# Performance work log

Hardware: AMD Instinct MI355X
Metric: run time of the kernel (lower is better)

## Reference

```python
import jax, jax.numpy as jnp
import numpy as np

B, L, D = 512, 200, 128
N_ITEMS = 50001
T_STEPS = 4
TAU = 2.0
STEP = 1
V_TH = 1.0
SG_ALPHA = 4.0  # spikingjelly default surrogate.Sigmoid alpha


@jax.custom_vjp
def spike(x):
    return (x >= 0.0).astype(x.dtype)

def _spike_fwd(x):
    return spike(x), x

def _spike_bwd(x, g):
    s = jax.nn.sigmoid(SG_ALPHA * x)
    return (g * SG_ALPHA * s * (1.0 - s),)

spike.defvjp(_spike_fwd, _spike_bwd)


def lif_multistep(x):
    """Multi-step LIF (hard reset to 0, detach_reset). x: [T, ...] -> spikes [T, ...]."""
    def step(v, xt):
        v = v + (xt - v) / TAU  # charge (v_reset = 0)
        s = spike(v - V_TH)
        v = v - jax.lax.stop_gradient(s) * v  # hard reset, detached spike
        return v, s
    v0 = jnp.zeros_like(x[0])
    _, spikes = jax.lax.scan(step, v0, x)
    return spikes


def layernorm(x, g, b, eps=1e-5):
    m = x.mean(-1, keepdims=True)
    v = x.var(-1, keepdims=True)
    return (x - m) / jnp.sqrt(v + eps) * g + b


def _build_session_graphs(rng):
    lens = rng.integers(50, L + 1, size=B)
    item_seq = np.zeros((B, L), dtype=np.int64)
    for b in range(B):
        item_seq[b, :lens[b]] = rng.integers(1, N_ITEMS, size=lens[b])
    alias = np.zeros((B, L), dtype=np.int64)
    items = np.zeros((B, L), dtype=np.int64)
    A = np.zeros((B, L, 2 * L), dtype=np.float32)
    for b in range(B):
        u = item_seq[b]
        node = np.unique(u)  # sorted
        items[b, :len(node)] = node
        alias[b] = np.searchsorted(node, u)
        uA = np.zeros((L, L), dtype=np.float32)
        for i in range(L - 1):
            if u[i + 1] == 0:
                break
            r = np.searchsorted(node, u[i])
            c = np.searchsorted(node, u[i + 1])
            uA[r, c] = 1.0
        sin = uA.sum(0); sin[sin == 0] = 1.0
        sout = uA.sum(1); sout[sout == 0] = 1.0
        A[b, :, :L] = (uA / sin).T          # u_A_in.T
        A[b, :, L:] = ((uA.T / sout)).T     # u_A_out.T
    mask = item_seq > 0
    return A, alias, items, mask, lens.astype(np.int64)


def setup_inputs() -> dict:
    rng = np.random.default_rng(0)
    A, alias, items, mask, lens = _build_session_graphs(rng)
    stdv = 1.0 / np.sqrt(D)
    key = jax.random.key(0)
    ks = jax.random.split(key, 24)
    u = lambda k, shape: jax.random.uniform(k, shape, jnp.float32, -stdv, stdv)
    item_emb = u(ks[0], (N_ITEMS, D)).at[0].set(0.0)  # padding_idx=0
    return {
        "A": jnp.asarray(A),
        "alias_inputs": jnp.asarray(alias),
        "items": jnp.asarray(items),
        "mask": jnp.asarray(mask),
        "item_seq_len": jnp.asarray(lens),
        "item_emb": item_emb,
        "W_in": u(ks[1], (D, D)), "b_in": u(ks[2], (D,)),
        "W_out": u(ks[3], (D, D)), "b_out": u(ks[4], (D,)),
        "w_ih": u(ks[5], (3 * D, 2 * D)), "w_hh": u(ks[6], (3 * D, D)),
        "b_ih": u(ks[7], (3 * D,)), "b_hh": u(ks[8], (3 * D,)),
        "b_iah": u(ks[9], (D,)), "b_ioh": u(ks[10], (D,)),
        "W1": u(ks[11], (D, D)), "W2": u(ks[12], (D, D)),
        "W3": u(ks[13], (1, D)), "Wt": u(ks[14], (D, 2 * D)),
        "g_q": u(ks[15], (D,)), "beta_q": u(ks[16], (D,)),
        "g_sh": u(ks[17], (2 * D,)), "beta_sh": u(ks[18], (2 * D,)),
    }


def _forward(A, alias_inputs, items, mask, item_seq_len, item_emb,
             W_in, b_in, W_out, b_out, w_ih, w_hh, b_ih, b_hh, b_iah, b_ioh,
             W1, W2, W3, Wt, g_q, beta_q, g_sh, beta_sh):
    hidden = item_emb[items]  # [B,L,D]
    for _ in range(STEP):
        ein = hidden @ W_in.T + b_in
        eout = hidden @ W_out.T + b_out
        input_in = jnp.einsum('bij,bjd->bid', A[:, :, :L], ein) + b_iah
        input_out = jnp.einsum('bij,bjd->bid', A[:, :, L:], eout) + b_ioh
        inputs = jnp.concatenate([input_in, input_out], axis=-1)  # [B,L,2D]
        gi = inputs @ w_ih.T + b_ih  # [B,L,3D]
        gh = hidden @ w_hh.T + b_hh
        i_r, i_i, i_n = jnp.split(gi, 3, axis=-1)
        h_r, h_i, h_n = jnp.split(gh, 3, axis=-1)
        r = jax.nn.sigmoid(i_r + h_r)
        z = jax.nn.sigmoid(i_i + h_i)
        n = jnp.tanh(i_n + r * h_n)
        hidden = (1.0 - z) * hidden + z * n
    seq_hidden = jnp.take_along_axis(hidden, alias_inputs[..., None], axis=1)  # [B,L,D]
    ht = jnp.take_along_axis(seq_hidden, (item_seq_len - 1)[:, None, None], axis=1)[:, 0]  # [B,D]
    Qb = (ht @ W1.T)[:, None, :] + seq_hidden @ W2.T  # [B,L,D]
    Q = jnp.broadcast_to(Qb[None], (T_STEPS, B, L, D))
    Qs = lif_multistep(layernorm(Q, g_q, beta_q))
    alpha = Qs @ W3.T  # [T,B,L,1]
    mf = mask.astype(alpha.dtype)
    a = jnp.sum(alpha * seq_hidden[None] * mf[None, :, :, None], axis=2)  # [T,B,D]
    ht_T = jnp.broadcast_to(ht[None], (T_STEPS, B, D))
    sh = jnp.concatenate([a, ht_T], axis=-1)  # [T,B,2D]
    sh = layernorm(lif_multistep(sh), g_sh, beta_sh)
    return (sh @ Wt.T).mean(0)  # [B,D]


def reference(A, alias_inputs, items, mask, item_seq_len, item_emb,
              W_in, b_in, W_out, b_out, w_ih, w_hh, b_ih, b_hh, b_iah, b_ioh,
              W1, W2, W3, Wt, g_q, beta_q, g_sh, beta_sh):
    return _forward(A, alias_inputs, items, mask, item_seq_len, item_emb,
                    W_in, b_in, W_out, b_out, w_ih, w_hh, b_ih, b_hh, b_iah, b_ioh,
                    W1, W2, W3, Wt, g_q, beta_q, g_sh, beta_sh)
```

## Files before the change

kernel.cpp:

```cpp
#include <hip/hip_runtime.h>
#include <hip/hip_bf16.h>
#include <cstdint>
#include <cstddef>

#define B_ 512
#define L_ 200
#define D_ 128
#define M_ (B_*L_)
#define T_ 4

typedef short bf16x8 __attribute__((ext_vector_type(8)));
typedef unsigned short u16x8 __attribute__((ext_vector_type(8)));
typedef float f32x4 __attribute__((ext_vector_type(4)));

__device__ __forceinline__ float bf2f(unsigned short u){
  union { unsigned int i; float f; } c; c.i = ((unsigned int)u)<<16; return c.f;
}
__device__ __forceinline__ unsigned short f2bf(float f){
  union { float f; unsigned int i; } c; c.f = f;
  unsigned int r = c.i + 0x7FFFu + ((c.i>>16)&1u);
  return (unsigned short)(r>>16);
}
__device__ __forceinline__ float wsum(float v){
  #pragma unroll
  for (int m=1;m<64;m<<=1) v += __shfl_xor(v, m, 64);
  return v;
}
__device__ __forceinline__ void gload_lds16(const void* g, void* l){
  __builtin_amdgcn_global_load_lds(
      (const __attribute__((address_space(1))) void*)g,
      (__attribute__((address_space(3))) void*)l, 16, 0, 0);
}

__global__ __launch_bounds__(256)
void gemm_bt(const unsigned short* __restrict__ A, int lda,
             const unsigned short* __restrict__ Bt, int ldb,
             const float* __restrict__ bias,
             unsigned short* __restrict__ C, int ldc, int K,
             const int* __restrict__ mlimit)
{
  const int m0 = blockIdx.y * 128;
  if (mlimit && m0 >= *mlimit) return;
  __shared__ __align__(16) short sAs[2][128*32];
  __shared__ __align__(16) short sBs[2][128*32];
  const int tid = threadIdx.x;
  const int n0 = blockIdx.x * 128;
  const int lane = tid & 63;
  const int w = tid >> 6;
  const int wr = (w>>1)*64, wc = (w&1)*64;

  f32x4 acc[4][4];
  #pragma unroll
  for (int i=0;i<4;i++)
    #pragma unroll
    for (int j=0;j<4;j++) acc[i][j] = (f32x4){0.f,0.f,0.f,0.f};

  const int c1 = tid, c2 = tid + 256;
  const int r1 = c1>>2, s1 = c1&3, k1 = ((s1 ^ ((r1>>1)&3))&3)<<3;
  const int r2 = c2>>2, s2 = c2&3, k2 = ((s2 ^ ((r2>>1)&3))&3)<<3;
  const int fr = lane & 15;
  const int fq = lane >> 4;
  const int fk = ((fq ^ ((fr>>1)&3))&3)<<3;

  auto stage = [&](int t){
    const int buf = t & 1, ks = t << 5;
    gload_lds16(A  + (size_t)(m0 + r1)*lda + ks + k1, sAs[buf] + (size_t)c1*8);
    gload_lds16(A  + (size_t)(m0 + r2)*lda + ks + k2, sAs[buf] + (size_t)c2*8);
    gload_lds16(Bt + (size_t)(n0 + r1)*ldb + ks + k1, sBs[buf] + (size_t)c1*8);
    gload_lds16(Bt + (size_t)(n0 + r2)*ldb + ks + k2, sBs[buf] + (size_t)c2*8);
  };
  const int nT = K >> 5;
  stage(0);
  __syncthreads();
  for (int t=0; t<nT; ++t){
    if (t+1 < nT) stage(t+1);
    const short* a_ = sAs[t&1];
    const short* b_ = sBs[t&1];
    bf16x8 af[4], bfr[4];
    #pragma unroll
    for (int i=0;i<4;i++){
      af[i]  = *(const bf16x8*)(a_ + (wr + i*16 + fr)*32 + fk);
      bfr[i] = *(const bf16x8*)(b_ + (wc + i*16 + fr)*32 + fk);
    }
    #pragma unroll
    for (int i=0;i<4;i++)
      #pragma unroll
      for (int j=0;j<4;j++)
        acc[i][j] = __builtin_amdgcn_mfma_f32_16x16x32_bf16(af[i], bfr[j], acc[i][j], 0,0,0);
    __syncthreads();
  }

  const int orow = fq<<2;
  #pragma unroll
  for (int i=0;i<4;i++){
    #pragma unroll
    for (int j=0;j<4;j++){
      const int gn = n0 + wc + j*16 + fr;
      const float bv = bias ? bias[gn] : 0.f;
      #pragma unroll
      for (int v=0;v<4;v++){
        const int gm = m0 + wr + i*16 + orow + v;
        C[(size_t)gm*ldc + gn] = f2bf(acc[i][j][v] + bv);
      }
    }
  }
}

__global__ __launch_bounds__(128)
void k_prepW(const float* __restrict__ w_ih, const float* __restrict__ w_hh,
             const float* __restrict__ W_in, const float* __restrict__ W_out,
             const float* __restrict__ b_in, const float* __restrict__ b_out,
             const float* __restrict__ b_ih, const float* __restrict__ b_hh,
             const float* __restrict__ b_iah, const float* __restrict__ b_ioh,
             unsigned short* __restrict__ Wbig, float* __restrict__ biasBase,
             float* __restrict__ uIn, float* __restrict__ uOut)
{
  const int p = blockIdx.x, t = threadIdx.x;
  const int dim = p>>2, g = p&3;
  const int row = (g==0) ? dim : (g==1) ? 128+dim : 256+dim;
  const bool has_ih = (g!=3), has_hh = (g!=2);
  __shared__ float wl[128], wrg[128], red[3][128];
  wl[t]  = has_ih ? w_ih[(size_t)row*256 + t]       : 0.f;
  wrg[t] = has_ih ? w_ih[(size_t)row*256 + 128 + t] : 0.f;
  __syncthreads();
  float cin = 0.f, cout = 0.f;
  if (has_ih) {
    for (int m=0;m<128;m++){
      cin  += wl[m]  * W_in [m*128 + t];
      cout += wrg[m] * W_out[m*128 + t];
    }
  }
  Wbig[(size_t)p*384 +       t] = f2bf(cin);
  Wbig[(size_t)p*384 + 128 + t] = f2bf(cout);
  Wbig[(size_t)p*384 + 256 + t] = f2bf(has_hh ? w_hh[(size_t)row*128 + t] : 0.f);
  red[0][t] = wl[t]*b_iah[t] + wrg[t]*b_ioh[t];
  red[1][t] = wl[t]*b_in[t];
  red[2][t] = wrg[t]*b_out[t];
  __syncthreads();
  if (t == 0) {
    float v=0.f, ui=0.f, uo=0.f;
    for (int k=0;k<128;k++){ v += red[0][k]; ui += red[1][k]; uo += red[2][k]; }
    float bb;
    if (g==0)      bb = b_ih[dim]     + b_hh[dim]     + v;
    else if (g==1) bb = b_ih[128+dim] + b_hh[128+dim] + v;
    else if (g==2) bb = b_ih[256+dim] + v;
    else           bb = b_hh[256+dim];
    biasBase[p] = bb;
    uIn[p]  = has_ih ? ui : 0.f;
    uOut[p] = has_ih ? uo : 0.f;
  }
}

__global__ __launch_bounds__(256)
void k_prepSmall(const float* __restrict__ W1, const float* __restrict__ W2,
                 unsigned short* __restrict__ w1b, unsigned short* __restrict__ w2b)
{
  const int i = blockIdx.x*256 + threadIdx.x;
  if (i < 16384) { w1b[i] = f2bf(W1[i]); w2b[i] = f2bf(W2[i]); }
}

__global__ __launch_bounds__(64)
void k_nb(const int* __restrict__ alias, const int* __restrict__ lens,
          int* __restrict__ nb)
{
  const int b = blockIdx.x, lane = threadIdx.x;
  const int len = lens[b];
  int m = 0;
  for (int l=lane; l<len; l+=64) m = max(m, alias[b*L_ + l]);
  #pragma unroll
  for (int o=1;o<64;o<<=1) m = max(m, __shfl_xor(m, o, 64));
  if (lane==0) nb[b] = m + 1;
}

__global__ __launch_bounds__(512)
void k_scan(const int* __restrict__ nb, const int* __restrict__ lens,
            int* __restrict__ nbase, int* __restrict__ vbase)
{
  __shared__ int A[2][512], Bv[2][512];
  const int t = threadIdx.x;
  const int a0 = nb[t], b0 = lens[t];
  A[0][t] = a0; Bv[0][t] = b0;
  __syncthreads();
  int cur = 0;
  for (int off=1; off<512; off<<=1){
    const int nxt = cur^1;
    A[nxt][t]  = A[cur][t]  + (t>=off ? A[cur][t-off]  : 0);
    Bv[nxt][t] = Bv[cur][t] + (t>=off ? Bv[cur][t-off] : 0);
    __syncthreads();
    cur = nxt;
  }
  nbase[t] = A[cur][t] - a0;
  vbase[t] = Bv[cur][t] - b0;
  if (t==511){ nbase[512] = A[cur][511]; vbase[512] = Bv[cur][511]; }
}

__global__ __launch_bounds__(1024)
void k_aggemb(const int* __restrict__ alias, const int* __restrict__ items,
              const int* __restrict__ lens, const float* __restrict__ emb,
              const int* __restrict__ nb, const int* __restrict__ nbase,
              unsigned short* __restrict__ X3, unsigned char* __restrict__ cf)
{
  const int b = blockIdx.x, tid = threadIdx.x;
  __shared__ unsigned short hl[L_*128];
  __shared__ int al[L_], it[L_];
  __shared__ unsigned bmIn[L_*8], bmOut[L_*8];
  if (tid < L_) { al[tid] = alias[b*L_ + tid]; it[tid] = items[b*L_ + tid]; }
  for (int i=tid; i<L_*8; i+=1024){ bmIn[i]=0u; bmOut[i]=0u; }
  __syncthreads();
  const int len = lens[b], nB = nb[b], base = nbase[b];
  if (tid < len-1) {
    const int r = al[tid], c = al[tid+1];
    atomicOr(&bmIn[c*8 + (r>>5)],  1u<<(r&31));
    atomicOr(&bmOut[r*8 + (c>>5)], 1u<<(c&31));
  }
  const int rr = tid>>5, cc = (tid&31)<<2;
  for (int s=0; s<nB; s+=32) {
    const int j = s + rr;
    if (j < nB) {
      const float4 v = *(const float4*)(emb + (size_t)it[j]*128 + cc);
      ushort4 o; o.x=f2bf(v.x); o.y=f2bf(v.y); o.z=f2bf(v.z); o.w=f2bf(v.w);
      *(ushort4*)(hl + j*128 + cc) = o;
      *(ushort4*)(X3 + (size_t)(base + j)*384 + 256 + cc) = o;
    }
  }
  __syncthreads();
  const int g = tid >> 7, d = tid & 127;
  for (int s=0; s<nB; s+=8) {
    const int i = s + g;
    if (i < nB) {
      float si=0.f, so=0.f; int ci=0, co=0;
      #pragma unroll
      for (int wd=0; wd<8; ++wd) {
        unsigned word = bmIn[i*8+wd];
        while (word) { int j = __ffs(word)-1; word &= word-1u;
          si += bf2f(hl[(wd*32+j)*128 + d]); ci++; }
        word = bmOut[i*8+wd];
        while (word) { int j = __ffs(word)-1; word &= word-1u;
          so += bf2f(hl[(wd*32+j)*128 + d]); co++; }
      }
      unsigned short* xr = X3 + (size_t)(base + i)*384;
      xr[d]       = f2bf(si / (float)(ci>0?ci:1));
      xr[128 + d] = f2bf(so / (float)(co>0?co:1));
      if (d == 0) cf[base + i] = (unsigned char)((ci>0?1:0) | (co>0?2:0));
    }
  }
}

__global__ __launch_bounds__(512)
void k_gates_gru(const unsigned short* __restrict__ X3,
                 const unsigned short* __restrict__ Wbig,
                 const float* __restrict__ biasBase,
                 const float* __restrict__ uIn,
                 const float* __restrict__ uOut,
                 const unsigned char* __restrict__ cf,
                 unsigned short* __restrict__ hidden,
                 const int* __restrict__ mlimit)
{
  const int m0 = blockIdx.y * 128;
  if (m0 >= *mlimit) return;
  __shared__ __align__(16) short sA[2][128*32];
  __shared__ __align__(16) short sB[2][256*32];
  const int tid = threadIdx.x;
  const int p0 = blockIdx.x * 256;
  const int lane = tid & 63;
  const int w = tid >> 6;
  const int wr  = (w>>2)*64;
  const int wcp = (w&3)*64;
  const int fr = lane & 15;
  const int fq = lane >> 4;
  const int fk = ((fq ^ ((fr>>1)&3))&3)<<3;

  f32x4 acc[4][4];
  #pragma unroll
  for (int i=0;i<4;i++)
    #pragma unroll
    for (int j=0;j<4;j++) acc[i][j] = (f32x4){0.f,0.f,0.f,0.f};

  const int ra = tid>>2, sa_ = tid&3, ka = ((sa_ ^ ((ra>>1)&3))&3)<<3;
  const int c1 = tid + 512, rb1 = c1>>2, sb1 = c1&3, kb1 = ((sb1 ^ ((rb1>>1)&3))&3)<<3;

  auto stage = [&](int t){
    const int buf = t & 1, ks = t << 5;
    gload_lds16(X3   + (size_t)(m0 + ra )*384 + ks + ka , sA[buf] + (size_t)tid*8);
    gload_lds16(Wbig + (size_t)(p0 + ra )*384 + ks + ka , sB[buf] + (size_t)tid*8);
    gload_lds16(Wbig + (size_t)(p0 + rb1)*384 + ks + kb1, sB[buf] + (size_t)(c1-512)*8 + 512*8);
  };
  stage(0);
  __syncthreads();
  for (int t=0; t<12; ++t){
    if (t < 11) stage(t+1);
    const short* a_ = sA[t&1];
    const short* b_ = sB[t&1];
    bf16x8 af[4], bfr[4];
    #pragma unroll
    for (int i=0;i<4;i++){
      af[i]  = *(const bf16x8*)(a_ + (wr  + i*16 + fr)*32 + fk);
      bfr[i] = *(const bf16x8*)(b_ + (wcp + i*16 + fr)*32 + fk);
    }
    #pragma unroll
    for (int i=0;i<4;i++)
      #pragma unroll
      for (int j=0;j<4;j++)
        acc[i][j] = __builtin_amdgcn_mfma_f32_16x16x32_bf16(af[i], bfr[j], acc[i][j], 0,0,0);
    __syncthreads();
  }

  const bool q0b = (lane & 1), q1b = (lane & 2);
  #pragma unroll
  for (int j=0;j<4;j++){
    const int dim = (p0>>2) + (w&3)*16 + j*4 + ((lane>>2)&3);
    const float4 bb = *(const float4*)(biasBase + dim*4);
    const float4 bi = *(const float4*)(uIn  + dim*4);
    const float4 bo = *(const float4*)(uOut + dim*4);
    #pragma unroll
    for (int i=0;i<4;i++){
      const float a0=acc[i][j][0], a1=acc[i][j][1], a2=acc[i][j][2], a3=acc[i][j][3];
      const float t0=__shfl_xor(a0,1), t1=__shfl_xor(a1,1), t2=__shfl_xor(a2,1), t3=__shfl_xor(a3,1);
      const float s0 = q0b? t1:a0, s1 = q0b? a1:t0, s2 = q0b? t3:a2, s3 = q0b? a3:t2;
      const float u0=__shfl_xor(s0,2), u1=__shfl_xor(s1,2), u2=__shfl_xor(s2,2), u3=__shfl_xor(s3,2);
      float G0 = q1b? u2:s0, G1 = q1b? u3:s1, G2 = q1b? s2:u0, G3 = q1b? s3:u1;
      const int row = m0 + wr + i*16 + fq*4 + (lane&3);
      const unsigned c = cf[row];
      const float fi = (c&1) ? 1.f : 0.f, fo = (c&2) ? 1.f : 0.f;
      G0 += bb.x + fi*bi.x + fo*bo.x;
      G1 += bb.y + fi*bi.y + fo*bo.y;
      G2 += bb.z + fi*bi.z + fo*bo.z;
      G3 += bb.w;
      const float h = bf2f(X3[(size_t)row*384 + 256 + dim]);
      const float r = 1.f/(1.f+__expf(-G0));
      const float z = 1.f/(1.f+__expf(-G1));
      const float x = G2 + r*G3;
      const float n = 1.f - 2.f/(__expf(2.f*x)+1.f);
      hidden[(size_t)row*128 + dim] = f2bf((1.f-z)*h + z*n);
    }
  }
}

__global__ __launch_bounds__(256)
void k_gather(const unsigned short* __restrict__ hidden,
              const int* __restrict__ alias, const int* __restrict__ lens,
              const int* __restrict__ nbase, const int* __restrict__ vbase,
              unsigned short* __restrict__ seqv, unsigned short* __restrict__ htb)
{
  const int idx = blockIdx.x*256 + threadIdx.x;
  const int row = idx >> 4, d8 = (idx & 15) << 3;
  const int b = row / L_, l = row - b*L_;
  const int len = lens[b];
  if (l >= len) return;
  u16x8 v = *(const u16x8*)(hidden + (size_t)(nbase[b] + alias[row])*128 + d8);
  *(u16x8*)(seqv + (size_t)(vbase[b] + l)*128 + d8) = v;
  if (l == len-1) *(u16x8*)(htb + (size_t)b*128 + d8) = v;
}

__global__ __launch_bounds__(1024)
void k_attn(const unsigned short* __restrict__ Q0, const unsigned short* __restrict__ htW1,
            const unsigned short* __restrict__ seqv, const int* __restrict__ lens,
            const int* __restrict__ vbase,
            const float* __restrict__ g_q, const float* __restrict__ beta_q,
            const float* __restrict__ W3, float* __restrict__ a_out)
{
  const int b = blockIdx.x, tid = threadIdx.x;
  const int w = tid>>6, lane = tid&63;
  __shared__ float a_acc[16][T_][128];
  for (int i=tid; i<16*T_*128; i+=1024) ((float*)a_acc)[i] = 0.f;
  const float h0 = bf2f(htW1[b*128 + lane]), h1 = bf2f(htW1[b*128 + lane + 64]);
  const float gq0 = g_q[lane], gq1 = g_q[lane+64];
  const float bq0 = beta_q[lane], bq1 = beta_q[lane+64];
  const float w30 = W3[lane], w31 = W3[lane+64];
  const int len = lens[b], vb = vbase[b];
  __syncthreads();
  for (int l = w; l < len; l += 16) {
    const size_t row = (size_t)(vb + l);
    const float q0 = bf2f(Q0[row*128 + lane]) + h0;
    const float q1 = bf2f(Q0[row*128 + lane + 64]) + h1;
    const float m = wsum(q0+q1) * (1.f/128.f);
    const float d0 = q0-m, d1 = q1-m;
    const float var = wsum(d0*d0 + d1*d1) * (1.f/128.f);
    const float inv = rsqrtf(var + 1e-5f);
    const float x0 = d0*inv*gq0 + bq0;
    const float x1 = d1*inv*gq1 + bq1;
    const float sh0 = bf2f(seqv[row*128+lane]), sh1 = bf2f(seqv[row*128+lane+64]);
    float v0=0.f, v1=0.f;
    #pragma unroll
    for (int t=0;t<T_;t++){
      v0 = 0.5f*(v0+x0); v1 = 0.5f*(v1+x1);
      const float s0 = (v0>=1.f)?1.f:0.f, s1 = (v1>=1.f)?1.f:0.f;
      v0 -= s0*v0; v1 -= s1*v1;
      const float alpha = wsum(s0*w30 + s1*w31);
      a_acc[w][t][lane] += alpha*sh0; a_acc[w][t][lane+64] += alpha*sh1;
    }
  }
  __syncthreads();
  for (int i=tid; i<T_*128; i+=1024){
    const int t = i>>7, d = i&127;
    float s = 0.f;
    #pragma unroll
    for (int p=0;p<16;p++) s += a_acc[p][t][d];
    a_out[((size_t)t*B_ + b)*128 + d] = s;
  }
}

__global__ __launch_bounds__(256)
void k_final(const float* __restrict__ a_in, const unsigned short* __restrict__ hidden,
             const int* __restrict__ alias, const int* __restrict__ lens,
             const int* __restrict__ nbase,
             const float* __restrict__ g_sh, const float* __restrict__ beta_sh,
             const float* __restrict__ Wt, float* __restrict__ out)
{
  const int b = blockIdx.x, tid = threadIdx.x;
  const int w = tid>>6, lane = tid&63;
  __shared__ float ys[256];
  __shared__ float part[T_][4];
  const int len = lens[b];
  float xh = 0.f;
  if (tid >= 128) {
    const int al = alias[b*L_ + len - 1];
    xh = bf2f(hidden[((size_t)(nbase[b] + al))*128 + (tid-128)]);
  }
  float v = 0.f; float sp[T_];
  #pragma unroll
  for (int t=0;t<T_;t++){
    const float x = (tid<128) ? a_in[((size_t)t*B_ + b)*128 + tid] : xh;
    v = 0.5f*(v + x);
    const float s = (v>=1.f)?1.f:0.f;
    v -= s*v;
    sp[t] = s;
  }
  #pragma unroll
  for (int t=0;t<T_;t++){
    const float r = wsum(sp[t]);
    if (lane==0) part[t][w] = r;
  }
  __syncthreads();
  float acc4 = 0.f;
  #pragma unroll
  for (int t=0;t<T_;t++){
    const float k = part[t][0]+part[t][1]+part[t][2]+part[t][3];
    const float mean = k * (1.f/256.f);
    const float varr = mean - mean*mean;
    const float inv = rsqrtf(varr + 1e-5f);
    acc4 += (sp[t]-mean)*inv;
  }
  ys[tid] = acc4*g_sh[tid] + 4.f*beta_sh[tid];
  __syncthreads();
  if (tid < 128) {
    float acc = 0.f;
    const float4* wr4 = (const float4*)(Wt + (size_t)tid*256);
    const float4* ys4 = (const float4*)ys;
    #pragma unroll 8
    for (int k=0;k<64;k++){
      const float4 wv = wr4[k], yv = ys4[k];
      acc += wv.x*yv.x + wv.y*yv.y + wv.z*yv.z + wv.w*yv.w;
    }
    out[(size_t)b*128 + tid] = acc*0.25f;
  }
}

extern "C" void kernel_launch(void* const* d_in, const int* in_sizes, int n_in,
                              void* d_out, int out_size, void* d_ws, size_t ws_size,
                              hipStream_t stream)
{
  const int*   alias  = (const int*)d_in[1];
  const int*   items  = (const int*)d_in[2];
  const int*   lens   = (const int*)d_in[4];
  const float* emb    = (const float*)d_in[5];
  const float* W_in   = (const float*)d_in[6];
  const float* b_in   = (const float*)d_in[7];
  const float* W_out  = (const float*)d_in[8];
  const float* b_out  = (const float*)d_in[9];
  const float* w_ih   = (const float*)d_in[10];
  const float* w_hh   = (const float*)d_in[11];
  const float* b_ih   = (const float*)d_in[12];
  const float* b_hh   = (const float*)d_in[13];
  const float* b_iah  = (const float*)d_in[14];
  const float* b_ioh  = (const float*)d_in[15];
  const float* W1     = (const float*)d_in[16];
  const float* W2     = (const float*)d_in[17];
  const float* W3     = (const float*)d_in[18];
  const float* Wt     = (const float*)d_in[19];
  const float* g_q    = (const float*)d_in[20];
  const float* beta_q = (const float*)d_in[21];
  const float* g_sh   = (const float*)d_in[22];
  const float* beta_sh= (const float*)d_in[23];

  char* ws = (char*)d_ws;
  size_t off = 0;
  auto alloc = [&](size_t bytes)->void* {
    void* p = ws + off; off += (bytes + 255) & ~(size_t)255; return p;
  };
  unsigned short* X3    = (unsigned short*)alloc((size_t)M_*384*2);
  unsigned short* hidden= (unsigned short*)alloc((size_t)M_*128*2);
  unsigned short* seqv  = (unsigned short*)alloc((size_t)M_*128*2);
  unsigned short* Q0c   = (unsigned short*)alloc((size_t)M_*128*2);
  unsigned short* htb   = (unsigned short*)alloc((size_t)B_*128*2);
  unsigned short* htW1  = (unsigned short*)alloc((size_t)B_*128*2);
  float*          a_buf = (float*)alloc((size_t)T_*B_*128*4);
  unsigned short* Wbig  = (unsigned short*)alloc((size_t)512*384*2);
  unsigned short* w1b   = (unsigned short*)alloc(16384*2);
  unsigned short* w2b   = (unsigned short*)alloc(16384*2);
  float*          biasBase = (float*)alloc(512*4);
  float*          uIn   = (float*)alloc(512*4);
  float*          uOut  = (float*)alloc(512*4);
  unsigned char*  cf    = (unsigned char*)alloc(M_);
  int*            nb    = (int*)alloc(512*4);
  int*            nbase = (int*)alloc(513*4);
  int*            vbase = (int*)alloc(513*4);
  if (off > ws_size) return;

  k_prepW<<<512,128,0,stream>>>(w_ih,w_hh,W_in,W_out,b_in,b_out,b_ih,b_hh,
                                b_iah,b_ioh,Wbig,biasBase,uIn,uOut);
  k_prepSmall<<<64,256,0,stream>>>(W1,W2,w1b,w2b);
  k_nb<<<B_,64,0,stream>>>(alias, lens, nb);
  k_scan<<<1,512,0,stream>>>(nb, lens, nbase, vbase);
  k_aggemb<<<B_,1024,0,stream>>>(alias, items, lens, emb, nb, nbase, X3, cf);
  k_gates_gru<<<dim3(2,800),512,0,stream>>>(X3, Wbig, biasBase, uIn, uOut, cf,
                                            hidden, nbase+512);
  k_gather<<<M_*16/256,256,0,stream>>>(hidden, alias, lens, nbase, vbase, seqv, htb);
  gemm_bt<<<dim3(1,4),256,0,stream>>>(htb, 128, w1b, 128, nullptr, htW1, 128, 128, nullptr);
  gemm_bt<<<dim3(1,800),256,0,stream>>>(seqv, 128, w2b, 128, nullptr, Q0c, 128, 128, vbase+512);
  k_attn<<<B_,1024,0,stream>>>(Q0c, htW1, seqv, lens, vbase, g_q, beta_q, W3, a_buf);
  k_final<<<B_,256,0,stream>>>(a_buf, hidden, alias, lens, nbase, g_sh, beta_sh, Wt, (float*)d_out);
}
```

Before: 199.6 us.

## Fuse Q0 GEMM with layernorm/LIF epilogue and triple-buffer GRU GEMM

The W2 GEMM over seqv now computes the layernorm, LIF spikes and alpha projection in its epilogue, so the bf16 Q0 intermediate is never written or reread. The old per-batch attention kernel becomes a light weighted-sum kernel that reads the per-row alpha values. Supporting this, the gather kernel records each row's batch index. Separately, the GRU gates GEMM moves from double to triple-buffered LDS loads with explicit vmcnt waits and one barrier per k-step, to overlap loads with MFMA work. The cost is more LDS per block, an extra alpha buffer in global memory, and hand-written waitcnt logic that must exactly match how many loads are in flight.

```diff
diff --git a/kernel.cpp b/kernel.cpp
--- a/kernel.cpp
+++ b/kernel.cpp
@@ -24,6 +24,11 @@
 __device__ __forceinline__ float wsum(float v){
   #pragma unroll
   for (int m=1;m<64;m<<=1) v += __shfl_xor(v, m, 64);
+  return v;
+}
+__device__ __forceinline__ float rsum16(float v){
+  #pragma unroll
+  for (int m=1;m<16;m<<=1) v += __shfl_xor(v, m, 64);
   return v;
 }
 __device__ __forceinline__ void gload_lds16(const void* g, void* l){
@@ -258,8 +263,8 @@
 {
   const int m0 = blockIdx.y * 128;
   if (m0 >= *mlimit) return;
-  __shared__ __align__(16) short sA[2][128*32];
-  __shared__ __align__(16) short sB[2][256*32];
+  __shared__ __align__(16) short sA[3*128*32];
+  __shared__ __align__(16) short sB[3*256*32];
   const int tid = threadIdx.x;
   const int p0 = blockIdx.x * 256;
   const int lane = tid & 63;
@@ -280,17 +285,20 @@
   const int c1 = tid + 512, rb1 = c1>>2, sb1 = c1&3, kb1 = ((sb1 ^ ((rb1>>1)&3))&3)<<3;
 
   auto stage = [&](int t){
-    const int buf = t & 1, ks = t << 5;
-    gload_lds16(X3   + (size_t)(m0 + ra )*384 + ks + ka , sA[buf] + (size_t)tid*8);
-    gload_lds16(Wbig + (size_t)(p0 + ra )*384 + ks + ka , sB[buf] + (size_t)tid*8);
-    gload_lds16(Wbig + (size_t)(p0 + rb1)*384 + ks + kb1, sB[buf] + (size_t)(c1-512)*8 + 512*8);
+    const int buf = t % 3, ks = t << 5;
+    gload_lds16(X3   + (size_t)(m0 + ra )*384 + ks + ka , sA + buf*4096 + (size_t)tid*8);
+    gload_lds16(Wbig + (size_t)(p0 + ra )*384 + ks + ka , sB + buf*8192 + (size_t)tid*8);
+    gload_lds16(Wbig + (size_t)(p0 + rb1)*384 + ks + kb1, sB + buf*8192 + 4096 + (size_t)tid*8);
   };
-  stage(0);
-  __syncthreads();
+  stage(0); stage(1);
   for (int t=0; t<12; ++t){
-    if (t < 11) stage(t+1);
-    const short* a_ = sA[t&1];
-    const short* b_ = sB[t&1];
+    if (t < 11) { asm volatile("s_waitcnt vmcnt(3)" ::: "memory"); }
+    else        { asm volatile("s_waitcnt vmcnt(0)" ::: "memory"); }
+    __builtin_amdgcn_s_barrier();
+    __builtin_amdgcn_sched_barrier(0);
+    if (t+2 < 12) stage(t+2);
+    const short* a_ = sA + (t%3)*4096;
+    const short* b_ = sB + (t%3)*8192;
     bf16x8 af[4], bfr[4];
     #pragma unroll
     for (int i=0;i<4;i++){
@@ -302,7 +310,6 @@
       #pragma unroll
       for (int j=0;j<4;j++)
         acc[i][j] = __builtin_amdgcn_mfma_f32_16x16x32_bf16(af[i], bfr[j], acc[i][j], 0,0,0);
-    __syncthreads();
   }
 
   const bool q0b = (lane & 1), q1b = (lane & 2);
@@ -340,63 +347,154 @@
 void k_gather(const unsigned short* __restrict__ hidden,
               const int* __restrict__ alias, const int* __restrict__ lens,
               const int* __restrict__ nbase, const int* __restrict__ vbase,
-              unsigned short* __restrict__ seqv, unsigned short* __restrict__ htb)
+              unsigned short* __restrict__ seqv, unsigned short* __restrict__ htb,
+              int* __restrict__ rowb)
 {
   const int idx = blockIdx.x*256 + threadIdx.x;
   const int row = idx >> 4, d8 = (idx & 15) << 3;
   const int b = row / L_, l = row - b*L_;
   const int len = lens[b];
   if (l >= len) return;
+  const int vrow = vbase[b] + l;
   u16x8 v = *(const u16x8*)(hidden + (size_t)(nbase[b] + alias[row])*128 + d8);
-  *(u16x8*)(seqv + (size_t)(vbase[b] + l)*128 + d8) = v;
+  *(u16x8*)(seqv + (size_t)vrow*128 + d8) = v;
   if (l == len-1) *(u16x8*)(htb + (size_t)b*128 + d8) = v;
-}
-
-__global__ __launch_bounds__(1024)
-void k_attn(const unsigned short* __restrict__ Q0, const unsigned short* __restrict__ htW1,
-            const unsigned short* __restrict__ seqv, const int* __restrict__ lens,
-            const int* __restrict__ vbase,
-            const float* __restrict__ g_q, const float* __restrict__ beta_q,
-            const float* __restrict__ W3, float* __restrict__ a_out)
+  if ((idx & 15) == 0) rowb[vrow] = b;
+}
+
+__global__ __launch_bounds__(256)
+void k_q0attn(const unsigned short* __restrict__ seqv,
+              const unsigned short* __restrict__ w2b,
+              const unsigned short* __restrict__ htW1,
+              const int* __restrict__ rowb,
+              const float* __restrict__ g_q, const float* __restrict__ beta_q,
+              const float* __restrict__ W3, float* __restrict__ alphaBuf,
+              const int* __restrict__ mlimit)
+{
+  const int m0 = blockIdx.x * 128;
+  const int Mv = *mlimit;
+  if (m0 >= Mv) return;
+  __shared__ __align__(16) short sA[3*128*32];
+  __shared__ __align__(16) short sB[3*128*32];
+  const int tid = threadIdx.x;
+  const int lane = tid & 63;
+  const int w = tid >> 6;
+  const int wr = w*32;
+  const int fr = lane & 15;
+  const int fq = lane >> 4;
+  const int fk = ((fq ^ ((fr>>1)&3))&3)<<3;
+
+  f32x4 acc[2][8];
+  #pragma unroll
+  for (int i=0;i<2;i++)
+    #pragma unroll
+    for (int j=0;j<8;j++) acc[i][j] = (f32x4){0.f,0.f,0.f,0.f};
+
+  const int c1 = tid, c2 = tid + 256;
+  const int r1 = c1>>2, s1 = c1&3, k1 = ((s1 ^ ((r1>>1)&3))&3)<<3;
+  const int r2 = c2>>2, s2 = c2&3, k2 = ((s2 ^ ((r2>>1)&3))&3)<<3;
+
+  auto stage = [&](int t){
+    const int buf = t % 3, ks = t << 5;
+    gload_lds16(seqv + (size_t)(m0 + r1)*128 + ks + k1, sA + buf*4096 + (size_t)c1*8);
+    gload_lds16(seqv + (size_t)(m0 + r2)*128 + ks + k2, sA + buf*4096 + (size_t)c2*8);
+    gload_lds16(w2b  + (size_t)r1*128 + ks + k1,        sB + buf*4096 + (size_t)c1*8);
+    gload_lds16(w2b  + (size_t)r2*128 + ks + k2,        sB + buf*4096 + (size_t)c2*8);
+  };
+  stage(0); stage(1);
+  for (int t=0; t<4; ++t){
+    if (t < 3) { asm volatile("s_waitcnt vmcnt(4)" ::: "memory"); }
+    else       { asm volatile("s_waitcnt vmcnt(0)" ::: "memory"); }
+    __builtin_amdgcn_s_barrier();
+    __builtin_amdgcn_sched_barrier(0);
+    if (t+2 < 4) stage(t+2);
+    const short* a_ = sA + (t%3)*4096;
+    const short* b_ = sB + (t%3)*4096;
+    bf16x8 af[2], bfr[8];
+    #pragma unroll
+    for (int i=0;i<2;i++)
+      af[i]  = *(const bf16x8*)(a_ + (wr + i*16 + fr)*32 + fk);
+    #pragma unroll
+    for (int j=0;j<8;j++)
+      bfr[j] = *(const bf16x8*)(b_ + (j*16 + fr)*32 + fk);
+    #pragma unroll
+    for (int i=0;i<2;i++)
+      #pragma unroll
+      for (int j=0;j<8;j++)
+        acc[i][j] = __builtin_amdgcn_mfma_f32_16x16x32_bf16(af[i], bfr[j], acc[i][j], 0,0,0);
+  }
+
+  const int colB = lane & 15;
+  float gc[8], bc[8], w3c[8];
+  #pragma unroll
+  for (int j=0;j<8;j++){
+    const int col = j*16 + colB;
+    gc[j] = g_q[col]; bc[j] = beta_q[col]; w3c[j] = W3[col];
+  }
+  #pragma unroll
+  for (int i=0;i<2;i++){
+    #pragma unroll
+    for (int v=0;v<4;v++){
+      const int row = m0 + wr + i*16 + fq*4 + v;
+      const bool valid = row < Mv;
+      const int b = valid ? rowb[row] : 0;
+      const unsigned short* htr = htW1 + (size_t)b*128;
+      float xv[8]; float pm = 0.f;
+      #pragma unroll
+      for (int j=0;j<8;j++){
+        xv[j] = acc[i][j][v] + bf2f(htr[j*16 + colB]);
+        pm += xv[j];
+      }
+      const float m = rsum16(pm) * (1.f/128.f);
+      float pv = 0.f;
+      #pragma unroll
+      for (int j=0;j<8;j++){ const float dd = xv[j]-m; pv += dd*dd; }
+      const float inv = rsqrtf(rsum16(pv)*(1.f/128.f) + 1e-5f);
+      #pragma unroll
+      for (int j=0;j<8;j++) xv[j] = (xv[j]-m)*inv*gc[j] + bc[j];
+      float vm[8] = {0,0,0,0,0,0,0,0};
+      #pragma unroll
+      for (int t=0;t<T_;t++){
+        float pa = 0.f;
+        #pragma unroll
+        for (int j=0;j<8;j++){
+          vm[j] = 0.5f*(vm[j]+xv[j]);
+          const float s = (vm[j]>=1.f)?1.f:0.f;
+          vm[j] -= s*vm[j];
+          pa += s*w3c[j];
+        }
+        pa = rsum16(pa);
+        if (colB==0 && valid) alphaBuf[(size_t)t*M_ + row] = pa;
+      }
+    }
+  }
+}
+
+__global__ __launch_bounds__(256)
+void k_attnsum(const float* __restrict__ alphaBuf,
+               const unsigned short* __restrict__ seqv,
+               const int* __restrict__ lens, const int* __restrict__ vbase,
+               float* __restrict__ a_out)
 {
   const int b = blockIdx.x, tid = threadIdx.x;
-  const int w = tid>>6, lane = tid&63;
-  __shared__ float a_acc[16][T_][128];
-  for (int i=tid; i<16*T_*128; i+=1024) ((float*)a_acc)[i] = 0.f;
-  const float h0 = bf2f(htW1[b*128 + lane]), h1 = bf2f(htW1[b*128 + lane + 64]);
-  const float gq0 = g_q[lane], gq1 = g_q[lane+64];
-  const float bq0 = beta_q[lane], bq1 = beta_q[lane+64];
-  const float w30 = W3[lane], w31 = W3[lane+64];
+  const int d = tid & 127, half = tid >> 7;
   const int len = lens[b], vb = vbase[b];
-  __syncthreads();
-  for (int l = w; l < len; l += 16) {
-    const size_t row = (size_t)(vb + l);
-    const float q0 = bf2f(Q0[row*128 + lane]) + h0;
-    const float q1 = bf2f(Q0[row*128 + lane + 64]) + h1;
-    const float m = wsum(q0+q1) * (1.f/128.f);
-    const float d0 = q0-m, d1 = q1-m;
-    const float var = wsum(d0*d0 + d1*d1) * (1.f/128.f);
-    const float inv = rsqrtf(var + 1e-5f);
-    const float x0 = d0*inv*gq0 + bq0;
-    const float x1 = d1*inv*gq1 + bq1;
-    const float sh0 = bf2f(seqv[row*128+lane]), sh1 = bf2f(seqv[row*128+lane+64]);
-    float v0=0.f, v1=0.f;
-    #pragma unroll
-    for (int t=0;t<T_;t++){
-      v0 = 0.5f*(v0+x0); v1 = 0.5f*(v1+x1);
-      const float s0 = (v0>=1.f)?1.f:0.f, s1 = (v1>=1.f)?1.f:0.f;
-      v0 -= s0*v0; v1 -= s1*v1;
-      const float alpha = wsum(s0*w30 + s1*w31);
-      a_acc[w][t][lane] += alpha*sh0; a_acc[w][t][lane+64] += alpha*sh1;
-    }
-  }
-  __syncthreads();
-  for (int i=tid; i<T_*128; i+=1024){
-    const int t = i>>7, d = i&127;
-    float s = 0.f;
-    #pragma unroll
-    for (int p=0;p<16;p++) s += a_acc[p][t][d];
-    a_out[((size_t)t*B_ + b)*128 + d] = s;
+  float a0=0.f, a1=0.f, a2=0.f, a3=0.f;
+  for (int l = half; l < len; l += 2){
+    const int row = vb + l;
+    const float sh = bf2f(seqv[(size_t)row*128 + d]);
+    a0 += alphaBuf[row]*sh;
+    a1 += alphaBuf[(size_t)M_ + row]*sh;
+    a2 += alphaBuf[(size_t)2*M_ + row]*sh;
+    a3 += alphaBuf[(size_t)3*M_ + row]*sh;
+  }
+  __shared__ float red[2][T_][128];
+  red[half][0][d]=a0; red[half][1][d]=a1; red[half][2][d]=a2; red[half][3][d]=a3;
+  __syncthreads();
+  if (half==0){
+    #pragma unroll
+    for (int t=0;t<T_;t++)
+      a_out[((size_t)t*B_ + b)*128 + d] = red[0][t][d] + red[1][t][d];
   }
 }
 
@@ -491,7 +589,8 @@
   unsigned short* X3    = (unsigned short*)alloc((size_t)M_*384*2);
   unsigned short* hidden= (unsigned short*)alloc((size_t)M_*128*2);
   unsigned short* seqv  = (unsigned short*)alloc((size_t)M_*128*2);
-  unsigned short* Q0c   = (unsigned short*)alloc((size_t)M_*128*2);
+  float*          alphaB= (float*)alloc((size_t)T_*M_*4);
+  int*            rowb  = (int*)alloc((size_t)M_*4);
   unsigned short* htb   = (unsigned short*)alloc((size_t)B_*128*2);
   unsigned short* htW1  = (unsigned short*)alloc((size_t)B_*128*2);
   float*          a_buf = (float*)alloc((size_t)T_*B_*128*4);
@@ -515,9 +614,12 @@
   k_aggemb<<<B_,1024,0,stream>>>(alias, items, lens, emb, nb, nbase, X3, cf);
   k_gates_gru<<<dim3(2,800),512,0,stream>>>(X3, Wbig, biasBase, uIn, uOut, cf,
                                             hidden, nbase+512);
-  k_gather<<<M_*16/256,256,0,stream>>>(hidden, alias, lens, nbase, vbase, seqv, htb);
+  k_gather<<<M_*16/256,256,0,stream>>>(hidden, alias, lens, nbase, vbase,
+                                       seqv, htb, rowb);
   gemm_bt<<<dim3(1,4),256,0,stream>>>(htb, 128, w1b, 128, nullptr, htW1, 128, 128, nullptr);
-  gemm_bt<<<dim3(1,800),256,0,stream>>>(seqv, 128, w2b, 128, nullptr, Q0c, 128, 128, vbase+512);
-  k_attn<<<B_,1024,0,stream>>>(Q0c, htW1, seqv, lens, vbase, g_q, beta_q, W3, a_buf);
-  k_final<<<B_,256,0,stream>>>(a_buf, hidden, alias, lens, nbase, g_sh, beta_sh, Wt, (float*)d_out);
-}
+  k_q0attn<<<800,256,0,stream>>>(seqv, w2b, htW1, rowb, g_q, beta_q, W3,
+                                 alphaB, vbase+512);
+  k_attnsum<<<B_,256,0,stream>>>(alphaB, seqv, lens, vbase, a_buf);
+  k_final<<<B_,256,0,stream>>>(a_buf, hidden, alias, lens, nbase, g_sh, beta_sh,
+                               Wt, (float*)d_out);
+}
```

Result: slower. 207.5 us (+3.9%).
